# Performance work log

Hardware: AMD Instinct MI355X
Metric: run time of the kernel (lower is better)

Reference implementation:

```python
import jax, jax.numpy as jnp
import numpy as np

B, P, K, KS = 512, 64, 30, 4      # graphs, nodes per graph, sort-pool k, conv1d kernel
N, E, F, H = B * P, 524288, 128, 256
N_CLASSES = 10
L_OUT = K - KS + 1                 # 27, conv1d output length


def _sage(h, wl, wr, b, src, dst, inv_deg):
    # PyG SAGEConv (mean aggr): out = lin_l(mean_j x_j) + lin_r(x_i); bias only on lin_l
    agg = jax.ops.segment_sum(h[src], dst, num_segments=N) * inv_deg
    return jax.nn.relu(agg @ wl + b + h @ wr)


def setup_inputs() -> dict:
    key = jax.random.key(0)
    ks = jax.random.split(key, 32)
    x = jax.random.normal(ks[0], (N, F), jnp.float32)
    # intra-graph random edges (src -> dst aggregation)
    g = jax.random.randint(ks[1], (E,), 0, B)
    src = g * P + jax.random.randint(ks[2], (E,), 0, P)
    dst = g * P + jax.random.randint(ks[3], (E,), 0, P)
    edge_index = jnp.stack([src, dst]).astype(jnp.int32)
    batch = jnp.repeat(jnp.arange(B), P).astype(jnp.int32)  # sorted graph ids

    def lin(k, i, o):
        return jax.random.normal(k, (i, o), jnp.float32) / np.float32(np.sqrt(i))

    inp = {"x": x, "edge_index": edge_index, "batch": batch}
    dims = [(F, H), (H, H), (H, H), (H, H)]
    ki = 4
    for li, (i, o) in enumerate(dims):
        inp[f"sage{li}_wl"] = lin(ks[ki], i, o); ki += 1
        inp[f"sage{li}_wr"] = lin(ks[ki], i, o); ki += 1
        inp[f"sage{li}_b"] = jnp.zeros((o,), jnp.float32)
    inp["conv1d_w"] = jax.random.normal(ks[ki], (H, H, KS), jnp.float32) / np.float32(np.sqrt(H * KS)); ki += 1
    inp["conv1d_b"] = jnp.zeros((H,), jnp.float32)
    inp["lin1_w"] = lin(ks[ki], H * L_OUT, H); ki += 1
    inp["lin1_b"] = jnp.zeros((H,), jnp.float32)
    inp["lin2_w"] = lin(ks[ki], H, 128); ki += 1
    inp["lin2_b"] = jnp.zeros((128,), jnp.float32)
    inp["out_w"] = lin(ks[ki], 128, N_CLASSES); ki += 1
    inp["out_b"] = jnp.zeros((N_CLASSES,), jnp.float32)
    return inp


def reference(x, edge_index, batch,
              sage0_wl, sage0_wr, sage0_b,
              sage1_wl, sage1_wr, sage1_b,
              sage2_wl, sage2_wr, sage2_b,
              sage3_wl, sage3_wr, sage3_b,
              conv1d_w, conv1d_b, lin1_w, lin1_b,
              lin2_w, lin2_b, out_w, out_b):
    src, dst = edge_index[0], edge_index[1]
    deg = jax.ops.segment_sum(jnp.ones(src.shape, x.dtype), dst, num_segments=N)
    inv_deg = (1.0 / jnp.maximum(deg, 1.0))[:, None]

    h = jnp.nan_to_num(x, nan=0.0)
    h = _sage(h, sage0_wl, sage0_wr, sage0_b, src, dst, inv_deg)
    h = _sage(h, sage1_wl, sage1_wr, sage1_b, src, dst, inv_deg)
    h = _sage(h, sage2_wl, sage2_wr, sage2_b, src, dst, inv_deg)
    h = _sage(h, sage3_wl, sage3_wr, sage3_b, src, dst, inv_deg)  # [N, H]

    # SortAggregation(k=K): to dense batch, sort by last channel desc, top-k, zero-pad
    counts = jax.ops.segment_sum(jnp.ones(N, jnp.int32), batch, num_segments=B)
    offsets = jnp.cumsum(counts) - counts
    pos = jnp.arange(N) - offsets[batch]
    D = h.shape[1]
    dense = jnp.zeros((B, P, D), h.dtype).at[batch, pos].set(h)
    valid = jnp.zeros((B, P), bool).at[batch, pos].set(True)
    skey = jnp.where(valid, dense[..., -1], -jnp.inf)
    order = jnp.argsort(-skey, axis=1)[:, :K]                       # [B, K]
    topk = jnp.take_along_axis(dense, order[..., None], axis=1)     # [B, K, D]
    tvalid = jnp.take_along_axis(valid, order, axis=1)
    topk = jnp.where(tvalid[..., None], topk, 0.0)

    # x.view(B, K, -1).permute(0, 2, 1) -> [B, D, K]
    xc = topk.transpose(0, 2, 1)
    y = jax.lax.conv_general_dilated(xc, conv1d_w, (1,), 'VALID',
                                     dimension_numbers=('NCH', 'OIH', 'NCH'))
    y = jax.nn.relu(y + conv1d_b[None, :, None])                    # [B, H, L_OUT]
    y = y.reshape(B, -1)                                            # dropout is identity in eval
    y = jax.nn.relu(y @ lin1_w + lin1_b)
    y = jax.nn.relu(y @ lin2_w + lin2_b)
    return jax.nn.relu(y @ out_w + out_b)                           # [B, N_CLASSES]
```

## Files before the change

### kernel.cpp

```cpp
#include <hip/hip_runtime.h>
#include <hip/hip_bf16.h>

#define NNODES 32768
#define NEDGES 524288
#define NGRAPH 512
#define PNODES 64
#define KTOP 30
#define FIN 128
#define HID 256
#define LOUT 27

#define C1F 4.8828125e-4f
#define C2F 2.384185791015625e-7f

using f16x8 = __attribute__((ext_vector_type(8))) _Float16;
using f16x4 = __attribute__((ext_vector_type(4))) _Float16;
using f32x4 = __attribute__((ext_vector_type(4))) float;
using f32x16 = __attribute__((ext_vector_type(16))) float;

#define GLDS(src, dst) __builtin_amdgcn_global_load_lds( \
    (const __attribute__((address_space(1))) void*)(src), \
    (__attribute__((address_space(3))) void*)(dst), 16, 0, 0)

__global__ void hist_kernel(const int* __restrict__ dst, int* __restrict__ counts) {
    int e = blockIdx.x * blockDim.x + threadIdx.x;
    if (e < NEDGES) atomicAdd(&counts[dst[e]], 1);
}

__global__ __launch_bounds__(1024) void scan_block_kernel(const int* __restrict__ counts,
        int* __restrict__ loc, int* __restrict__ partial) {
    int b = blockIdx.x, t = threadIdx.x;
    int i = b * 1024 + t;
    int v = counts[i];
    int lane = t & 63, w = t >> 6;
    int x = v;
    #pragma unroll
    for (int d = 1; d < 64; d <<= 1) { int y = __shfl_up(x, d, 64); if (lane >= d) x += y; }
    __shared__ int ws[16];
    if (lane == 63) ws[w] = x;
    __syncthreads();
    if (w == 0) {
        int s = (lane < 16) ? ws[lane] : 0;
        #pragma unroll
        for (int d = 1; d < 16; d <<= 1) { int y = __shfl_up(s, d, 64); if (lane >= d) s += y; }
        if (lane < 16) ws[lane] = s;
    }
    __syncthreads();
    int base = (w > 0) ? ws[w - 1] : 0;
    int incl = base + x;
    loc[i] = incl - v;
    if (t == 1023) partial[b] = incl;
}

__global__ __launch_bounds__(1024) void scan_fixup_kernel(const int* __restrict__ loc,
        const int* __restrict__ partial, const int* __restrict__ counts,
        int* __restrict__ offsets, int* __restrict__ cursor, float* __restrict__ invdeg) {
    int b = blockIdx.x, t = threadIdx.x;
    int i = b * 1024 + t;
    __shared__ int sbase;
    if (t == 0) { int s = 0; for (int j = 0; j < b; ++j) s += partial[j]; sbase = s; }
    __syncthreads();
    int o = loc[i] + sbase;
    offsets[i] = o;
    cursor[i] = o;
    invdeg[i] = 1.0f / fmaxf((float)counts[i], 1.0f);
}

__global__ void scatter_kernel(const int* __restrict__ src, const int* __restrict__ dst,
        int* __restrict__ cursor, int* __restrict__ ssrc) {
    int e = blockIdx.x * blockDim.x + threadIdx.x;
    if (e < NEDGES) {
        int d = dst[e];
        int p = atomicAdd(&cursor[d], 1);
        ssrc[p] = ((d & 63) << 6) | (src[e] & 63);
    }
}

__global__ void nan2num_split_kernel(const float* __restrict__ x,
        _Float16* __restrict__ oh, _Float16* __restrict__ ol, int n4) {
    int i = blockIdx.x * blockDim.x + threadIdx.x;
    if (i >= n4) return;
    float4 v = *(const float4*)(x + i * 4);
    float xs[4] = {v.x, v.y, v.z, v.w};
    f16x4 hh, ll;
    #pragma unroll
    for (int q = 0; q < 4; ++q) {
        float a = xs[q];
        a = (a != a) ? 0.f : a;
        _Float16 h = (_Float16)a;
        hh[q] = h;
        ll[q] = (_Float16)((a - (float)h) * 2048.0f);
    }
    *(f16x4*)(oh + (size_t)i * 4) = hh;
    *(f16x4*)(ol + (size_t)i * 4) = ll;
}

struct Prep8 {
    const float* src[8];
    _Float16* dh[8];
    _Float16* dl[8];
    int logK[8];
    int nelem[8];
    int rstride[8];
};

__global__ __launch_bounds__(256) void prep8_kernel(Prep8 p) {
    int y = blockIdx.y;
    int idx = blockIdx.x * 256 + threadIdx.x;
    if (idx >= p.nelem[y]) return;
    int lk = p.logK[y], K = 1 << lk;
    int n = idx >> lk, k = idx & (K - 1);
    float w = p.src[y][(size_t)k * 256 + n];
    _Float16 h = (_Float16)w;
    p.dh[y][(size_t)n * p.rstride[y] + k] = h;
    p.dl[y][(size_t)n * p.rstride[y] + k] = (_Float16)((w - (float)h) * 2048.0f);
}

__global__ __launch_bounds__(256) void prep_conv_kernel(const float* __restrict__ W,
        _Float16* __restrict__ b0, _Float16* __restrict__ b1) {
    int idx = blockIdx.x * 256 + threadIdx.x;
    int o = idx >> 10, k = idx & 1023;
    float w = W[(size_t)o * 1024 + (k & 255) * 4 + (k >> 8)];
    _Float16 h = (_Float16)w;
    b0[(size_t)o * 1024 + k] = h;
    b1[(size_t)o * 1024 + k] = (_Float16)((w - (float)h) * 2048.0f);
}

__global__ __launch_bounds__(256) void prep_lin1_kernel(const float* __restrict__ l1w,
        _Float16* __restrict__ wh, _Float16* __restrict__ wl_) {
    __shared__ float sh[64][65];
    int kb = blockIdx.x * 64;
    int nb = blockIdx.y * 64;
    int t = threadIdx.x;
    {
        int kk = t >> 2;
        int nc = (t & 3) * 16;
        int k = kb + kk, l = k >> 8, c = k & 255;
        const float* srow = l1w + (size_t)(c * 27 + l) * 256 + nb + nc;
        #pragma unroll
        for (int j = 0; j < 16; j += 4) {
            float4 v = *(const float4*)(srow + j);
            sh[kk][nc + j + 0] = v.x;
            sh[kk][nc + j + 1] = v.y;
            sh[kk][nc + j + 2] = v.z;
            sh[kk][nc + j + 3] = v.w;
        }
    }
    __syncthreads();
    {
        int nn = t >> 2;
        int kc = (t & 3) * 16;
        f16x8 oh[2], ol[2];
        #pragma unroll
        for (int j = 0; j < 16; ++j) {
            float x = sh[kc + j][nn];
            _Float16 h = (_Float16)x;
            oh[j >> 3][j & 7] = h;
            ol[j >> 3][j & 7] = (_Float16)((x - (float)h) * 2048.0f);
        }
        size_t o = (size_t)(nb + nn) * 6912 + kb + kc;
        *(f16x8*)(wh + o) = oh[0];
        *(f16x8*)(wh + o + 8) = oh[1];
        *(f16x8*)(wl_ + o) = ol[0];
        *(f16x8*)(wl_ + o + 8) = ol[1];
    }
}

template<int HIN>
__global__ __launch_bounds__(512, 4) void fused_sage2_kernel(
        const _Float16* __restrict__ hh, const _Float16* __restrict__ hl,
        const int* __restrict__ offsets, const int* __restrict__ counts,
        const int* __restrict__ ssrc, const float* __restrict__ invdeg,
        const _Float16* __restrict__ Wh, const _Float16* __restrict__ Wl_,
        const float* __restrict__ bias,
        _Float16* __restrict__ outh, _Float16* __restrict__ outl) {
    constexpr int NCH = HIN / 32;
    __shared__ __align__(16) _Float16 hp[2][NCH * 2048];
    __shared__ __align__(16) uint32_t Sw[4096];
    const int g = blockIdx.x, t = threadIdx.x;
    const int lane = t & 63, wave = t >> 6;
    const int l31 = lane & 31, hb = lane >> 5;
    const size_t gbase = (size_t)g * 64 * HIN;

    #pragma unroll
    for (int i = 0; i < 8; ++i) Sw[t + i * 512] = 0;

    {
        int a = lane >> 2, b = lane & 3;
        for (int u = wave; u < NCH * 8; u += 8) {
            int part = u & 1;
            int cs = u >> 1;
            int c = cs >> 2, stripe = cs & 3;
            int row = stripe * 16 + a;
            int o = b ^ ((row >> 1) & 3) ^ (c & 3);
            const _Float16* src = (part ? hl : hh) + gbase + (size_t)row * HIN + c * 32 + o * 8;
            GLDS(src, &hp[part][c * 2048 + stripe * 512]);
        }
    }

    const int gbeg = offsets[g * 64];
    const int gend = offsets[g * 64 + 63] + counts[g * 64 + 63];
    __syncthreads();

    for (int e = gbeg + t; e < gend; e += 512)
        atomicAdd(&Sw[ssrc[e] & 4095], 1u);
    __syncthreads();

    {
        int d = t >> 3, o = t & 7;
        float idg = invdeg[g * 64 + d];
        float v[8];
        #pragma unroll
        for (int j = 0; j < 8; ++j) v[j] = (float)Sw[(d << 6) + (o << 3) + j] * idg;
        __syncthreads();
        _Float16* Sp = (_Float16*)Sw;
        f16x8 s0, s1;
        #pragma unroll
        for (int j = 0; j < 8; ++j) {
            _Float16 h1 = (_Float16)v[j];
            s0[j] = h1;
            s1[j] = (_Float16)((v[j] - (float)h1) * 2048.0f);
        }
        int addr = (d << 6) + ((o ^ (d & 7)) << 3);
        *(f16x8*)&Sp[addr] = s0;
        *(f16x8*)&Sp[4096 + addr] = s1;
    }
    __syncthreads();

    const int col = (wave << 5) + l31;

    auto gemmKV = [&](const _Float16* __restrict__ Bh, const _Float16* __restrict__ Bl,
                      f32x16* a0, f32x16* a1) {
        #pragma unroll 2
        for (int c = 0; c < NCH; ++c) {
            #pragma unroll
            for (int h2 = 0; h2 < 2; ++h2) {
                f16x8 ah[2], al_[2];
                #pragma unroll
                for (int mi = 0; mi < 2; ++mi) {
                    int row = (mi << 5) + l31;
                    int slot = (2 * h2 + hb) ^ ((row >> 1) & 3) ^ (c & 3);
                    int addr = c * 2048 + (row << 5) + (slot << 3);
                    ah[mi] = *(const f16x8*)&hp[0][addr];
                    al_[mi] = *(const f16x8*)&hp[1][addr];
                }
                int ko = (c << 5) + (h2 << 4) + (hb << 3);
                f16x8 bh = *(const f16x8*)(Bh + ko);
                f16x8 bl = *(const f16x8*)(Bl + ko);
                #pragma unroll
                for (int mi = 0; mi < 2; ++mi) {
                    a0[mi] = __builtin_amdgcn_mfma_f32_32x32x16_f16(ah[mi], bh, a0[mi], 0, 0, 0);
                    a1[mi] = __builtin_amdgcn_mfma_f32_32x32x16_f16(al_[mi], bh, a1[mi], 0, 0, 0);
                    a1[mi] = __builtin_amdgcn_mfma_f32_32x32x16_f16(ah[mi], bl, a1[mi], 0, 0, 0);
                }
            }
        }
    };

    f32x16 acc0[2], acc1[2];
    acc0[0] = 0.f; acc0[1] = 0.f; acc1[0] = 0.f; acc1[1] = 0.f;
    gemmKV(Wh + (size_t)col * HIN, Wl_ + (size_t)col * HIN, acc0, acc1);
    f32x16 pf[2];
    pf[0] = acc0[0] + C1F * acc1[0];
    pf[1] = acc0[1] + C1F * acc1[1];

    f32x16 so0[2], so1[2];
    so0[0] = 0.f; so0[1] = 0.f; so1[0] = 0.f; so1[1] = 0.f;
    {
        const _Float16* Sp = (const _Float16*)Sw;
        #pragma unroll
        for (int kc = 0; kc < 4; ++kc) {
            float kv[4], sv[4];
            #pragma unroll
            for (int j = 0; j < 4; ++j) {
                float e0 = pf[(2 * kc) >> 2][((2 * kc) & 3) * 4 + j];
                float e1 = pf[(2 * kc + 1) >> 2][((2 * kc + 1) & 3) * 4 + j];
                kv[j] = hb ? e1 : e0;
                sv[j] = hb ? e0 : e1;
            }
            uint32_t kh[2], kl2[2], sh_[2], sl2[2];
            #pragma unroll
            for (int q = 0; q < 2; ++q) {
                union { uint32_t u; _Float16 f[2]; } H1, L1, H2, L2;
                #pragma unroll
                for (int j = 0; j < 2; ++j) {
                    float x = kv[q * 2 + j];
                    _Float16 h1 = (_Float16)x;
                    H1.f[j] = h1; L1.f[j] = (_Float16)((x - (float)h1) * 2048.0f);
                    float y = sv[q * 2 + j];
                    _Float16 h2 = (_Float16)y;
                    H2.f[j] = h2; L2.f[j] = (_Float16)((y - (float)h2) * 2048.0f);
                }
                kh[q] = H1.u; kl2[q] = L1.u; sh_[q] = H2.u; sl2[q] = L2.u;
            }
            uint32_t rh0 = (uint32_t)__shfl_xor((int)sh_[0], 32, 64);
            uint32_t rh1 = (uint32_t)__shfl_xor((int)sh_[1], 32, 64);
            uint32_t rl0 = (uint32_t)__shfl_xor((int)sl2[0], 32, 64);
            uint32_t rl1 = (uint32_t)__shfl_xor((int)sl2[1], 32, 64);
            union { uint32_t u[4]; f16x8 v; } bh_, bl_;
            bh_.u[0] = hb ? rh0 : kh[0];  bh_.u[1] = hb ? rh1 : kh[1];
            bh_.u[2] = hb ? kh[0] : rh0;  bh_.u[3] = hb ? kh[1] : rh1;
            bl_.u[0] = hb ? rl0 : kl2[0]; bl_.u[1] = hb ? rl1 : kl2[1];
            bl_.u[2] = hb ? kl2[0] : rl0; bl_.u[3] = hb ? kl2[1] : rl1;
            #pragma unroll
            for (int mi = 0; mi < 2; ++mi) {
                int row = (mi << 5) + l31;
                int soff = (row << 6) + (((2 * kc + hb) ^ (row & 7)) << 3);
                f16x8 s0f = *(const f16x8*)&Sp[soff];
                f16x8 s1f = *(const f16x8*)&Sp[4096 + soff];
                so0[mi] = __builtin_amdgcn_mfma_f32_32x32x16_f16(s0f, bh_.v, so0[mi], 0, 0, 0);
                so1[mi] = __builtin_amdgcn_mfma_f32_32x32x16_f16(s0f, bl_.v, so1[mi], 0, 0, 0);
                so1[mi] = __builtin_amdgcn_mfma_f32_32x32x16_f16(s1f, bh_.v, so1[mi], 0, 0, 0);
            }
        }
    }
    f32x16 sC[2];
    sC[0] = so0[0] + C1F * so1[0];
    sC[1] = so0[1] + C1F * so1[1];

    acc0[0] = 0.f; acc0[1] = 0.f; acc1[0] = 0.f; acc1[1] = 0.f;
    gemmKV(Wh + (size_t)(256 + col) * HIN, Wl_ + (size_t)(256 + col) * HIN, acc0, acc1);

    const float bb = bias[col];
    #pragma unroll
    for (int mi = 0; mi < 2; ++mi) {
        #pragma unroll
        for (int reg = 0; reg < 16; ++reg) {
            float v = sC[mi][reg] + acc0[mi][reg] + C1F * acc1[mi][reg] + bb;
            v = fmaxf(v, 0.f);
            int row = (mi << 5) + (reg & 3) + ((reg >> 2) << 3) + (hb << 2);
            _Float16 h1 = (_Float16)v;
            size_t o = (size_t)((g << 6) + row) * HID + col;
            outh[o] = h1;
            outl[o] = (_Float16)((v - (float)h1) * 2048.0f);
        }
    }
}

template<int NPROD, int CONV, int NPAIRS, int EPI>
__global__ __launch_bounds__(256, 2) void mfma_ps_kernel(
        const _Float16* __restrict__ A1h, const _Float16* __restrict__ A1l,
        const _Float16* __restrict__ A2h, const _Float16* __restrict__ A2l,
        const _Float16* __restrict__ B1h, const _Float16* __restrict__ B1l,
        const _Float16* __restrict__ B2h, const _Float16* __restrict__ B2l,
        const float* __restrict__ bias,
        _Float16* __restrict__ outh, _Float16* __restrict__ outl,
        float* __restrict__ Cpart,
        int lda, int K, int Nd, int nrb) {
    __shared__ _Float16 As[2][2][128 * 32];
    __shared__ _Float16 Bs[2][2][128 * 32];
    const int t = threadIdx.x;
    const int lane = t & 63, wave = t >> 6;
    const int wr = wave & 1, wc = wave >> 1;
    const int bid = blockIdx.x;
    const int rb = bid % nrb, cb = bid / nrb;
    const int row0 = rb * 128, col0 = cb * 128;
    const int l31 = lane & 31, hb = lane >> 5, x3 = l31 & 3;
    const int r16 = lane >> 2;
    const int qsrc8 = ((lane & 3) ^ (r16 & 3)) * 8;
    size_t aoffj[2], boffj[2];
    #pragma unroll
    for (int j = 0; j < 2; ++j) {
        int ar = row0 + wave * 32 + j * 16 + r16;
        aoffj[j] = CONV ? ((size_t)ar * 256 + (size_t)(ar / 27) * 768)
                        : (size_t)ar * (size_t)lda;
        boffj[j] = (size_t)(col0 + wave * 32 + j * 16 + r16) * (size_t)K;
    }
    int aroff[2], broff[2], slot8[2];
    #pragma unroll
    for (int mi = 0; mi < 2; ++mi) aroff[mi] = (wr * 64 + mi * 32 + l31) * 32;
    #pragma unroll
    for (int ni = 0; ni < 2; ++ni) broff[ni] = (wc * 64 + ni * 32 + l31) * 32;
    #pragma unroll
    for (int h = 0; h < 2; ++h) slot8[h] = ((2 * h + hb) ^ x3) * 8;

    const int KV = NPAIRS * K;
    const int kchunk = KV / gridDim.z;
    const int kv_lo = blockIdx.z * kchunk, kv_hi = kv_lo + kchunk;

    f32x16 acc0[2][2], acc1[2][2], acc2[2][2];
    #pragma unroll
    for (int i = 0; i < 2; ++i)
        #pragma unroll
        for (int j = 0; j < 2; ++j) { acc0[i][j] = 0.f; acc1[i][j] = 0.f; acc2[i][j] = 0.f; }

    auto stage = [&](int kv, int b) {
        int p = (NPAIRS == 2 && kv >= K) ? 1 : 0;
        int k = kv - p * K;
        const _Float16* __restrict__ sAh = p ? A2h : A1h;
        const _Float16* __restrict__ sAl = p ? A2l : A1l;
        const _Float16* __restrict__ sBh = p ? B2h : B1h;
        const _Float16* __restrict__ sBl = p ? B2l : B1l;
        #pragma unroll
        for (int j = 0; j < 2; ++j) {
            int ldsbase = (wave * 32 + j * 16) * 32;
            size_t ga = aoffj[j] + k + qsrc8;
            size_t gb = boffj[j] + k + qsrc8;
            GLDS(sAh + ga, &As[b][0][ldsbase]);
            GLDS(sAl + ga, &As[b][1][ldsbase]);
            GLDS(sBh + gb, &Bs[b][0][ldsbase]);
            GLDS(sBl + gb, &Bs[b][1][ldsbase]);
        }
    };

    stage(kv_lo, 0);
    __syncthreads();
    int b = 0;
    for (int kv = kv_lo; kv < kv_hi; kv += 32) {
        if (kv + 32 < kv_hi) stage(kv + 32, b ^ 1);
        #pragma unroll
        for (int h = 0; h < 2; ++h) {
            f16x8 af0[2], af1[2], bf0[2], bf1[2];
            #pragma unroll
            for (int mi = 0; mi < 2; ++mi) {
                af0[mi] = *(const f16x8*)&As[b][0][aroff[mi] + slot8[h]];
                af1[mi] = *(const f16x8*)&As[b][1][aroff[mi] + slot8[h]];
            }
            #pragma unroll
            for (int ni = 0; ni < 2; ++ni) {
                bf0[ni] = *(const f16x8*)&Bs[b][0][broff[ni] + slot8[h]];
                bf1[ni] = *(const f16x8*)&Bs[b][1][broff[ni] + slot8[h]];
            }
            #pragma unroll
            for (int mi = 0; mi < 2; ++mi)
                #pragma unroll
                for (int ni = 0; ni < 2; ++ni) {
                    acc0[mi][ni] = __builtin_amdgcn_mfma_f32_32x32x16_f16(af0[mi], bf0[ni], acc0[mi][ni], 0, 0, 0);
                    acc1[mi][ni] = __builtin_amdgcn_mfma_f32_32x32x16_f16(af1[mi], bf0[ni], acc1[mi][ni], 0, 0, 0);
                    acc1[mi][ni] = __builtin_amdgcn_mfma_f32_32x32x16_f16(af0[mi], bf1[ni], acc1[mi][ni], 0, 0, 0);
                    if (NPROD == 4)
                        acc2[mi][ni] = __builtin_amdgcn_mfma_f32_32x32x16_f16(af1[mi], bf1[ni], acc2[mi][ni], 0, 0, 0);
                }
        }
        b ^= 1;
        __syncthreads();
    }

    const int rquad = 4 * hb;
    #pragma unroll
    for (int ni = 0; ni < 2; ++ni) {
        int col = col0 + wc * 64 + ni * 32 + l31;
        float bb = (EPI == 0) ? bias[col] : 0.f;
        #pragma unroll
        for (int mi = 0; mi < 2; ++mi) {
            #pragma unroll
            for (int reg = 0; reg < 16; ++reg) {
                float v = acc0[mi][ni][reg] + C1F * acc1[mi][ni][reg];
                if (NPROD == 4) v += C2F * acc2[mi][ni][reg];
                int row = row0 + wr * 64 + mi * 32 + (reg & 3) + 8 * (reg >> 2) + rquad;
                if (EPI == 0) {
                    v = fmaxf(v + bb, 0.f);
                    _Float16 h = (_Float16)v;
                    size_t o = (size_t)row * Nd + col;
                    outh[o] = h;
                    outl[o] = (_Float16)((v - (float)h) * 2048.0f);
                } else {
                    size_t zb = (size_t)blockIdx.z * (size_t)(nrb * 128) * Nd;
                    Cpart[zb + (size_t)row * Nd + col] = v;
                }
            }
        }
    }
}

__global__ __launch_bounds__(256) void sortgather_kernel(const _Float16* __restrict__ hh,
        const _Float16* __restrict__ hl, _Float16* __restrict__ th, _Float16* __restrict__ tl) {
    __shared__ float vals[PNODES];
    __shared__ int ord[KTOP];
    int g = blockIdx.x, t = threadIdx.x;
    if (t < PNODES) {
        size_t idx = (size_t)(g * PNODES + t) * HID + (HID - 1);
        vals[t] = (float)hh[idx] + C1F * (float)hl[idx];
    }
    __syncthreads();
    if (t < PNODES) {
        float v = vals[t];
        int rank = 0;
        for (int j = 0; j < PNODES; ++j) {
            float vj = vals[j];
            rank += (vj > v) || (vj == v && j < t);
        }
        if (rank < KTOP) ord[rank] = g * PNODES + t;
    }
    __syncthreads();
    int c8 = (t & 31) * 8;
    for (int r = t >> 5; r < KTOP; r += 8) {
        size_t s = (size_t)ord[r] * HID + c8;
        size_t d = (size_t)(g * KTOP + r) * HID + c8;
        *(f16x8*)(th + d) = *(const f16x8*)(hh + s);
        *(f16x8*)(tl + d) = *(const f16x8*)(hl + s);
    }
}

__global__ void reduce_conv_kernel(const float* __restrict__ yb32,
        const float* __restrict__ b, _Float16* __restrict__ ybh, _Float16* __restrict__ ybl) {
    int i = blockIdx.x * 256 + threadIdx.x;
    float v = fmaxf(yb32[i] + yb32[i + 13824 * 256] + b[i & 255], 0.f);
    _Float16 h = (_Float16)v;
    ybh[i] = h;
    ybl[i] = (_Float16)((v - (float)h) * 2048.0f);
}

__global__ void reduce_lin1_kernel(const float* __restrict__ z1p,
        const float* __restrict__ b, float* __restrict__ z1) {
    int i = blockIdx.x * 256 + threadIdx.x;
    float s = b[i & 255];
    #pragma unroll
    for (int z = 0; z < 27; ++z) s += z1p[(size_t)z * 131072 + i];
    z1[i] = fmaxf(s, 0.f);
}

__global__ __launch_bounds__(256) void gemm64_kernel(
        const float* __restrict__ A, const float* __restrict__ B,
        const float* __restrict__ bias, float* __restrict__ C,
        int lda, int kend, int Nd) {
    __shared__ float As[16][64];
    __shared__ float Bs[16][64];
    const int tid = threadIdx.x;
    const int tx = tid & 15, ty = tid >> 4;
    const int la_r = tid >> 2, la_c = (tid & 3) << 2;
    const int lb_r = tid >> 4, lb_c = (tid & 15) << 2;
    const int row0 = blockIdx.x * 64, col0 = blockIdx.y * 64;
    const size_t aoff = (size_t)(row0 + la_r) * (size_t)lda;
    float acc[4][4] = {};
    for (int k0 = 0; k0 < kend; k0 += 16) {
        __syncthreads();
        float4 av = *(const float4*)(A + aoff + k0 + la_c);
        As[la_c + 0][la_r] = av.x;
        As[la_c + 1][la_r] = av.y;
        As[la_c + 2][la_r] = av.z;
        As[la_c + 3][la_r] = av.w;
        *(float4*)&Bs[lb_r][lb_c] = *(const float4*)(B + (size_t)(k0 + lb_r) * Nd + col0 + lb_c);
        __syncthreads();
        #pragma unroll
        for (int k = 0; k < 16; ++k) {
            float4 a = *(const float4*)&As[k][ty << 2];
            float4 b = *(const float4*)&Bs[k][tx << 2];
            acc[0][0] += a.x * b.x; acc[0][1] += a.x * b.y; acc[0][2] += a.x * b.z; acc[0][3] += a.x * b.w;
            acc[1][0] += a.y * b.x; acc[1][1] += a.y * b.y; acc[1][2] += a.y * b.z; acc[1][3] += a.y * b.w;
            acc[2][0] += a.z * b.x; acc[2][1] += a.z * b.y; acc[2][2] += a.z * b.z; acc[2][3] += a.z * b.w;
            acc[3][0] += a.w * b.x; acc[3][1] += a.w * b.y; acc[3][2] += a.w * b.z; acc[3][3] += a.w * b.w;
        }
    }
    #pragma unroll
    for (int i = 0; i < 4; ++i) {
        int row = row0 + (ty << 2) + i;
        #pragma unroll
        for (int j = 0; j < 4; ++j) {
            int col = col0 + (tx << 2) + j;
            C[(size_t)row * Nd + col] = fmaxf(acc[i][j] + bias[col], 0.f);
        }
    }
}

__global__ void out_kernel(const float* __restrict__ z2, const float* __restrict__ w,
        const float* __restrict__ b, float* __restrict__ out) {
    int idx = blockIdx.x * blockDim.x + threadIdx.x;
    if (idx < NGRAPH * 10) {
        int r = idx / 10, c = idx % 10;
        float s = b[c];
        for (int k = 0; k < 128; ++k) s += z2[r * 128 + k] * w[k * 10 + c];
        out[idx] = fmaxf(s, 0.f);
    }
}

extern "C" void kernel_launch(void* const* d_in, const int* in_sizes, int n_in,
                              void* d_out, int out_size, void* d_ws, size_t ws_size,
                              hipStream_t stream) {
    const float* x    = (const float*)d_in[0];
    const int*   edge = (const int*)d_in[1];
    const int*   esrc = edge;
    const int*   edst = edge + NEDGES;
    const float* wl[4] = {(const float*)d_in[3], (const float*)d_in[6], (const float*)d_in[9],  (const float*)d_in[12]};
    const float* wr[4] = {(const float*)d_in[4], (const float*)d_in[7], (const float*)d_in[10], (const float*)d_in[13]};
    const float* sb[4] = {(const float*)d_in[5], (const float*)d_in[8], (const float*)d_in[11], (const float*)d_in[14]};
    const float* convw = (const float*)d_in[15];
    const float* convb = (const float*)d_in[16];
    const float* l1w   = (const float*)d_in[17];
    const float* l1b   = (const float*)d_in[18];
    const float* l2w   = (const float*)d_in[19];
    const float* l2b   = (const float*)d_in[20];
    const float* ow    = (const float*)d_in[21];
    const float* ob    = (const float*)d_in[22];
    float* out = (float*)d_out;

    char* ws = (char*)d_ws;
    size_t off = 0;
    auto alloc = [&](size_t bytes) -> char* {
        char* p = ws + off;
        off = (off + bytes + 255) & ~(size_t)255;
        return p;
    };
    int*   counts  = (int*)alloc((size_t)NNODES * 4);
    int*   offsets = (int*)alloc((size_t)NNODES * 4);
    int*   cursor  = (int*)alloc((size_t)NNODES * 4);
    int*   loc     = (int*)alloc((size_t)NNODES * 4);
    int*   partial = (int*)alloc(32 * 4);
    float* invdeg  = (float*)alloc((size_t)NNODES * 4);
    int*   ssrc    = (int*)alloc((size_t)NEDGES * 4);
    _Float16* wch[4]; _Float16* wcl[4];
    for (int l = 0; l < 4; ++l) {
        size_t kb = (size_t)512 * (l ? HID : FIN) * 2;
        wch[l] = (_Float16*)alloc(kb);
        wcl[l] = (_Float16*)alloc(kb);
    }
    _Float16* cvh = (_Float16*)alloc((size_t)HID * 1024 * 2);
    _Float16* cvl = (_Float16*)alloc((size_t)HID * 1024 * 2);

    const size_t H0T = (size_t)NNODES * FIN * 2;
    const size_t AGT = (size_t)NNODES * HID * 2;
    const size_t TKT = (size_t)NGRAPH * KTOP * HID * 2;
    const size_t YBT = (size_t)NGRAPH * LOUT * HID * 2;
    const size_t YB32T = (size_t)2 * 13824 * 256 * 4;
    const size_t W1T = (size_t)HID * 6912 * 2;

    char* R1 = alloc(2 * H0T);
    char* R2 = alloc(2 * AGT);
    char* R3 = alloc(2 * AGT);
    char* R4 = alloc(2 * AGT);
    _Float16* h0h = (_Float16*)R1; _Float16* h0l = (_Float16*)(R1 + H0T);
    _Float16* tkh = (_Float16*)R1; _Float16* tkl = (_Float16*)(R1 + TKT);
    _Float16* hAh = (_Float16*)R3; _Float16* hAl = (_Float16*)(R3 + AGT);
    _Float16* ybh = (_Float16*)R2; _Float16* ybl_ = (_Float16*)(R2 + YBT);
    float* yb32 = (float*)(R2 + 2 * YBT);
    float* z1p  = (float*)(R2 + 2 * YBT);
    char* tail2 = R2 + 2 * YBT + YB32T;
    float* z1  = (float*)tail2;
    float* z2  = (float*)(tail2 + (size_t)NGRAPH * HID * 4);
    _Float16* w1h = (_Float16*)(tail2 + (size_t)NGRAPH * HID * 4 + (size_t)NGRAPH * 128 * 4 + 256);
    _Float16* w1l = (_Float16*)((char*)w1h + W1T);
    _Float16* hBh = (_Float16*)R4; _Float16* hBl = (_Float16*)(R4 + AGT);

    hipMemsetAsync(counts, 0, (size_t)NNODES * 4, stream);
    hist_kernel<<<NEDGES / 256, 256, 0, stream>>>(edst, counts);
    scan_block_kernel<<<NNODES / 1024, 1024, 0, stream>>>(counts, loc, partial);
    scan_fixup_kernel<<<NNODES / 1024, 1024, 0, stream>>>(loc, partial, counts, offsets, cursor, invdeg);
    scatter_kernel<<<NEDGES / 256, 256, 0, stream>>>(esrc, edst, cursor, ssrc);
    nan2num_split_kernel<<<(NNODES * FIN / 4) / 256, 256, 0, stream>>>(x, h0h, h0l, NNODES * FIN / 4);

    Prep8 p8;
    for (int l = 0; l < 4; ++l) {
        int K = l ? HID : FIN, lk = l ? 8 : 7;
        p8.src[2 * l] = wl[l];     p8.dh[2 * l] = wch[l];                 p8.dl[2 * l] = wcl[l];
        p8.src[2 * l + 1] = wr[l]; p8.dh[2 * l + 1] = wch[l] + 256 * K;  p8.dl[2 * l + 1] = wcl[l] + 256 * K;
        p8.logK[2 * l] = lk;     p8.nelem[2 * l] = 256 * K;     p8.rstride[2 * l] = K;
        p8.logK[2 * l + 1] = lk; p8.nelem[2 * l + 1] = 256 * K; p8.rstride[2 * l + 1] = K;
    }
    prep8_kernel<<<dim3(256, 8), 256, 0, stream>>>(p8);
    prep_conv_kernel<<<(HID * 1024) / 256, 256, 0, stream>>>(convw, cvh, cvl);

    fused_sage2_kernel<FIN><<<NGRAPH, 512, 0, stream>>>(
        h0h, h0l, offsets, counts, ssrc, invdeg, wch[0], wcl[0], sb[0], hAh, hAl);
    _Float16* hinh = hAh; _Float16* hinl = hAl;
    _Float16* hoth = hBh; _Float16* hotl = hBl;
    for (int l = 1; l < 4; ++l) {
        fused_sage2_kernel<HID><<<NGRAPH, 512, 0, stream>>>(
            hinh, hinl, offsets, counts, ssrc, invdeg, wch[l], wcl[l], sb[l], hoth, hotl);
        _Float16* t1 = hinh; hinh = hoth; hoth = t1;
        _Float16* t2 = hinl; hinl = hotl; hotl = t2;
    }

    sortgather_kernel<<<NGRAPH, 256, 0, stream>>>(hinh, hinl, tkh, tkl);
    prep_lin1_kernel<<<dim3(108, 4), 256, 0, stream>>>(l1w, w1h, w1l);

    mfma_ps_kernel<3, 1, 1, 1><<<dim3(108 * 2, 1, 2), 256, 0, stream>>>(
        tkh, tkl, nullptr, nullptr, cvh, cvl, nullptr, nullptr, nullptr, nullptr, nullptr, yb32, 256, 1024, HID, 108);
    reduce_conv_kernel<<<13824 * 256 / 256, 256, 0, stream>>>(yb32, convb, ybh, ybl_);

    mfma_ps_kernel<3, 0, 1, 1><<<dim3(4 * 2, 1, 27), 256, 0, stream>>>(
        ybh, ybl_, nullptr, nullptr, w1h, w1l, nullptr, nullptr, nullptr, nullptr, nullptr, z1p, 6912, 6912, HID, 4);
    reduce_lin1_kernel<<<NGRAPH * HID / 256, 256, 0, stream>>>(z1p, l1b, z1);

    gemm64_kernel<<<dim3(NGRAPH / 64, 128 / 64), 256, 0, stream>>>(z1, l2w, l2b, z2, HID, HID, 128);

    out_kernel<<<(NGRAPH * 10 + 255) / 256, 256, 0, stream>>>(z2, ow, ob, out);
}
```

Baseline: 481.1 us.

## Pre-swizzle SAGE weights for coalesced loads and stage outputs through LDS

The weight-prep kernel now writes the SAGE weights in a per-wave, per-MFMA-fragment order, so each lane's B-operand load in the fused SAGE kernel becomes one contiguous 16-byte read per wave step instead of strided row reads. The epilogue now writes results into a swizzled LDS tile and then stores 16-byte vectors per row to global memory, replacing scattered 2-byte stores. This aims to cut uncoalesced global traffic on both the weight loads and the output writes. In exchange it adds extra LDS round trips and barriers in the epilogue.

```diff
diff --git a/kernel.cpp b/kernel.cpp
--- a/kernel.cpp
+++ b/kernel.cpp
@@ -95,25 +95,29 @@
     *(f16x4*)(ol + (size_t)i * 4) = ll;
 }
 
-struct Prep8 {
+struct PrepSage {
     const float* src[8];
     _Float16* dh[8];
     _Float16* dl[8];
     int logK[8];
-    int nelem[8];
-    int rstride[8];
+    int part[8];
 };
 
-__global__ __launch_bounds__(256) void prep8_kernel(Prep8 p) {
+__global__ __launch_bounds__(256) void prep_sage_kernel(PrepSage p) {
     int y = blockIdx.y;
     int idx = blockIdx.x * 256 + threadIdx.x;
-    if (idx >= p.nelem[y]) return;
     int lk = p.logK[y], K = 1 << lk;
+    if (idx >= 256 * K) return;
     int n = idx >> lk, k = idx & (K - 1);
     float w = p.src[y][(size_t)k * 256 + n];
     _Float16 h = (_Float16)w;
-    p.dh[y][(size_t)n * p.rstride[y] + k] = h;
-    p.dl[y][(size_t)n * p.rstride[y] + k] = (_Float16)((w - (float)h) * 2048.0f);
+    int wv = n >> 5, l31 = n & 31;
+    int c = k >> 5, h2 = (k >> 4) & 1, hb = (k >> 3) & 1, j = k & 7;
+    int NCH = K >> 5;
+    size_t dst = (size_t)(wv * 2 + p.part[y]) * (size_t)(NCH * 1024)
+               + (size_t)(c * 2 + h2) * 512 + (size_t)(hb * 32 + l31) * 8 + j;
+    p.dh[y][dst] = h;
+    p.dl[y][dst] = (_Float16)((w - (float)h) * 2048.0f);
 }
 
 __global__ __launch_bounds__(256) void prep_conv_kernel(const float* __restrict__ W,
@@ -167,11 +171,11 @@
 }
 
 template<int HIN>
-__global__ __launch_bounds__(512, 4) void fused_sage2_kernel(
+__global__ __launch_bounds__(512, 4) void fused_sage3_kernel(
         const _Float16* __restrict__ hh, const _Float16* __restrict__ hl,
         const int* __restrict__ offsets, const int* __restrict__ counts,
         const int* __restrict__ ssrc, const float* __restrict__ invdeg,
-        const _Float16* __restrict__ Wh, const _Float16* __restrict__ Wl_,
+        const _Float16* __restrict__ Wsh, const _Float16* __restrict__ Wsl,
         const float* __restrict__ bias,
         _Float16* __restrict__ outh, _Float16* __restrict__ outl) {
     constexpr int NCH = HIN / 32;
@@ -229,8 +233,9 @@
 
     const int col = (wave << 5) + l31;
 
-    auto gemmKV = [&](const _Float16* __restrict__ Bh, const _Float16* __restrict__ Bl,
-                      f32x16* a0, f32x16* a1) {
+    auto gemmKV = [&](int part, f32x16* a0, f32x16* a1) {
+        const _Float16* __restrict__ Bh = Wsh + (size_t)((wave << 1) + part) * (size_t)(NCH * 1024);
+        const _Float16* __restrict__ Bl = Wsl + (size_t)((wave << 1) + part) * (size_t)(NCH * 1024);
         #pragma unroll 2
         for (int c = 0; c < NCH; ++c) {
             #pragma unroll
@@ -244,7 +249,7 @@
                     ah[mi] = *(const f16x8*)&hp[0][addr];
                     al_[mi] = *(const f16x8*)&hp[1][addr];
                 }
-                int ko = (c << 5) + (h2 << 4) + (hb << 3);
+                int ko = ((c << 1) + h2) * 512 + (lane << 3);
                 f16x8 bh = *(const f16x8*)(Bh + ko);
                 f16x8 bl = *(const f16x8*)(Bl + ko);
                 #pragma unroll
@@ -259,7 +264,7 @@
 
     f32x16 acc0[2], acc1[2];
     acc0[0] = 0.f; acc0[1] = 0.f; acc1[0] = 0.f; acc1[1] = 0.f;
-    gemmKV(Wh + (size_t)col * HIN, Wl_ + (size_t)col * HIN, acc0, acc1);
+    gemmKV(0, acc0, acc1);
     f32x16 pf[2];
     pf[0] = acc0[0] + C1F * acc1[0];
     pf[1] = acc0[1] + C1F * acc1[1];
@@ -319,21 +324,41 @@
     sC[1] = so0[1] + C1F * so1[1];
 
     acc0[0] = 0.f; acc0[1] = 0.f; acc1[0] = 0.f; acc1[1] = 0.f;
-    gemmKV(Wh + (size_t)(256 + col) * HIN, Wl_ + (size_t)(256 + col) * HIN, acc0, acc1);
+    gemmKV(1, acc0, acc1);
 
     const float bb = bias[col];
     #pragma unroll
-    for (int mi = 0; mi < 2; ++mi) {
-        #pragma unroll
-        for (int reg = 0; reg < 16; ++reg) {
-            float v = sC[mi][reg] + acc0[mi][reg] + C1F * acc1[mi][reg] + bb;
-            v = fmaxf(v, 0.f);
-            int row = (mi << 5) + (reg & 3) + ((reg >> 2) << 3) + (hb << 2);
-            _Float16 h1 = (_Float16)v;
-            size_t o = (size_t)((g << 6) + row) * HID + col;
-            outh[o] = h1;
-            outl[o] = (_Float16)((v - (float)h1) * 2048.0f);
-        }
+    for (int mi = 0; mi < 2; ++mi)
+        #pragma unroll
+        for (int reg = 0; reg < 16; ++reg)
+            sC[mi][reg] = fmaxf(sC[mi][reg] + acc0[mi][reg] + C1F * acc1[mi][reg] + bb, 0.f);
+
+    __syncthreads();
+    _Float16* eL = &hp[0][0];
+    #pragma unroll
+    for (int part = 0; part < 2; ++part) {
+        #pragma unroll
+        for (int mi = 0; mi < 2; ++mi) {
+            #pragma unroll
+            for (int reg = 0; reg < 16; ++reg) {
+                int row = (mi << 5) + (reg & 3) + ((reg >> 2) << 3) + (hb << 2);
+                int cx = col ^ ((((row >> 2) & 1) << 5) | ((row & 3) << 3));
+                float v = sC[mi][reg];
+                _Float16 h1 = (_Float16)v;
+                eL[(row << 8) + cx] = part ? (_Float16)((v - (float)h1) * 2048.0f) : h1;
+            }
+        }
+        __syncthreads();
+        _Float16* gout = part ? outl : outh;
+        #pragma unroll
+        for (int it = 0; it < 4; ++it) {
+            int i = (t << 3) + (it << 12);
+            int row = i >> 8, cc = i & 255;
+            int sx = cc ^ ((((row >> 2) & 1) << 5) | ((row & 3) << 3));
+            f16x8 v8 = *(const f16x8*)&eL[(row << 8) + sx];
+            *(f16x8*)(gout + (size_t)((g << 6) + row) * HID + cc) = v8;
+        }
+        if (part == 0) __syncthreads();
     }
 }
 
@@ -638,23 +663,23 @@
     scatter_kernel<<<NEDGES / 256, 256, 0, stream>>>(esrc, edst, cursor, ssrc);
     nan2num_split_kernel<<<(NNODES * FIN / 4) / 256, 256, 0, stream>>>(x, h0h, h0l, NNODES * FIN / 4);
 
-    Prep8 p8;
+    PrepSage ps;
     for (int l = 0; l < 4; ++l) {
-        int K = l ? HID : FIN, lk = l ? 8 : 7;
-        p8.src[2 * l] = wl[l];     p8.dh[2 * l] = wch[l];                 p8.dl[2 * l] = wcl[l];
-        p8.src[2 * l + 1] = wr[l]; p8.dh[2 * l + 1] = wch[l] + 256 * K;  p8.dl[2 * l + 1] = wcl[l] + 256 * K;
-        p8.logK[2 * l] = lk;     p8.nelem[2 * l] = 256 * K;     p8.rstride[2 * l] = K;
-        p8.logK[2 * l + 1] = lk; p8.nelem[2 * l + 1] = 256 * K; p8.rstride[2 * l + 1] = K;
-    }
-    prep8_kernel<<<dim3(256, 8), 256, 0, stream>>>(p8);
+        int lk = l ? 8 : 7;
+        ps.src[2 * l] = wl[l];     ps.dh[2 * l] = wch[l];     ps.dl[2 * l] = wcl[l];
+        ps.src[2 * l + 1] = wr[l]; ps.dh[2 * l + 1] = wch[l]; ps.dl[2 * l + 1] = wcl[l];
+        ps.logK[2 * l] = lk;     ps.part[2 * l] = 0;
+        ps.logK[2 * l + 1] = lk; ps.part[2 * l + 1] = 1;
+    }
+    prep_sage_kernel<<<dim3(256, 8), 256, 0, stream>>>(ps);
     prep_conv_kernel<<<(HID * 1024) / 256, 256, 0, stream>>>(convw, cvh, cvl);
 
-    fused_sage2_kernel<FIN><<<NGRAPH, 512, 0, stream>>>(
+    fused_sage3_kernel<FIN><<<NGRAPH, 512, 0, stream>>>(
         h0h, h0l, offsets, counts, ssrc, invdeg, wch[0], wcl[0], sb[0], hAh, hAl);
     _Float16* hinh = hAh; _Float16* hinl = hAl;
     _Float16* hoth = hBh; _Float16* hotl = hBl;
     for (int l = 1; l < 4; ++l) {
-        fused_sage2_kernel<HID><<<NGRAPH, 512, 0, stream>>>(
+        fused_sage3_kernel<HID><<<NGRAPH, 512, 0, stream>>>(
             hinh, hinl, offsets, counts, ssrc, invdeg, wch[l], wcl[l], sb[l], hoth, hotl);
         _Float16* t1 = hinh; hinh = hoth; hoth = t1;
         _Float16* t2 = hinl; hinl = hotl; hotl = t2;
```

Result: no change. 487.6 us (+1.3%).
